# Kernel optimization log

Hardware: AMD Instinct MI355X
Metric: run time of the kernel (lower is better)

Reference implementation:

```python
import jax, jax.numpy as jnp
import numpy as np

D_MODEL, N_LAYER, VOCAB = 1024, 4, 50280
D_INNER, D_STATE, D_CONV, DT_RANK = 2048, 16, 4, 64
B, L = 1, 1024
EPS = 1e-5


def _rmsnorm(x, w):
    var = jnp.mean(jnp.square(x), axis=-1, keepdims=True)
    return x * jax.lax.rsqrt(var + EPS) * w


def _selective_scan(u, dt, A, Bm, Cm, Dv):
    # u, dt: [b,l,d]; A: [d,n]; Bm, Cm: [b,l,n]; Dv: [d]
    dA = jnp.exp(dt[..., None] * A)                      # [b,l,d,n]
    dBu = dt[..., None] * Bm[:, :, None, :] * u[..., None]  # [b,l,d,n]

    def step(s, x):
        dA_t, dBu_t, C_t = x
        s = s * dA_t + dBu_t                             # [b,d,n]
        y = jnp.einsum('bdn,bn->bd', s, C_t)
        return s, y

    s0 = jnp.zeros((u.shape[0], u.shape[2], A.shape[1]), u.dtype)
    xs = (dA.transpose(1, 0, 2, 3), dBu.transpose(1, 0, 2, 3), Cm.transpose(1, 0, 2))
    _, ys = jax.lax.scan(step, s0, xs)                   # ys: [l,b,d]
    return ys.transpose(1, 0, 2) + u * Dv


def _mixer(x, in_w, cw, cb, xp_w, dt_w, dt_b, A_log, Dv, out_w):
    Lx = x.shape[1]
    xz = jnp.einsum('bld,ed->ble', x, in_w)              # [b,l,2*d_inner]
    xp, z = jnp.split(xz, 2, axis=-1)
    # causal depthwise conv1d, kernel size D_CONV
    xpad = jnp.pad(xp, ((0, 0), (D_CONV - 1, 0), (0, 0)))
    conv = cb + sum(xpad[:, k:k + Lx, :] * cw[:, k] for k in range(D_CONV))
    u = jax.nn.silu(conv)
    xdbl = jnp.einsum('bld,ed->ble', u, xp_w)            # [b,l,dt_rank+2n]
    dt_r = xdbl[..., :DT_RANK]
    Bm = xdbl[..., DT_RANK:DT_RANK + D_STATE]
    Cm = xdbl[..., DT_RANK + D_STATE:]
    dt = jax.nn.softplus(jnp.einsum('blr,dr->bld', dt_r, dt_w) + dt_b)
    A = -jnp.exp(A_log)
    y = _selective_scan(u, dt, A, Bm, Cm, Dv)
    y = y * jax.nn.silu(z)
    return jnp.einsum('bld,ed->ble', y, out_w)


def _forward(input_ids, embedding, norm_w, in_proj_w, conv_w, conv_b, x_proj_w,
             dt_proj_w, dt_proj_b, A_log, D, out_proj_w, norm_f_w):
    hidden = embedding[input_ids]                        # [b,l,d_model]
    residual = None
    for i in range(N_LAYER):
        residual = hidden if residual is None else hidden + residual
        x = _rmsnorm(residual, norm_w[i])
        hidden = _mixer(x, in_proj_w[i], conv_w[i], conv_b[i], x_proj_w[i],
                        dt_proj_w[i], dt_proj_b[i], A_log[i], D[i], out_proj_w[i])
    residual = hidden + residual
    hf = _rmsnorm(residual, norm_f_w)
    # lm_head weight is tied to embedding
    return jnp.einsum('bld,vd->blv', hf, embedding)


def setup_inputs() -> dict:
    key = jax.random.key(0)
    ks = jax.random.split(key, 8)
    s = 0.02
    return {
        'input_ids': jax.random.randint(ks[0], (B, L), 0, VOCAB),
        'embedding': jax.random.normal(ks[1], (VOCAB, D_MODEL), jnp.float32) * s,
        'norm_w': jnp.ones((N_LAYER, D_MODEL), jnp.float32),
        'in_proj_w': jax.random.normal(ks[2], (N_LAYER, 2 * D_INNER, D_MODEL), jnp.float32) * s,
        'conv_w': jax.random.normal(ks[3], (N_LAYER, D_INNER, D_CONV), jnp.float32) * s,
        'conv_b': jnp.zeros((N_LAYER, D_INNER), jnp.float32),
        'x_proj_w': jax.random.normal(ks[4], (N_LAYER, DT_RANK + 2 * D_STATE, D_INNER), jnp.float32) * s,
        'dt_proj_w': jax.random.normal(ks[5], (N_LAYER, D_INNER, DT_RANK), jnp.float32) * s,
        'dt_proj_b': jnp.full((N_LAYER, D_INNER), -4.6, jnp.float32),  # softplus ~= 0.01
        'A_log': jnp.tile(jnp.log(jnp.arange(1.0, D_STATE + 1.0, dtype=jnp.float32))[None, None, :],
                          (N_LAYER, D_INNER, 1)),
        'D': jnp.ones((N_LAYER, D_INNER), jnp.float32),
        'out_proj_w': jax.random.normal(ks[6], (N_LAYER, D_MODEL, D_INNER), jnp.float32) * s,
        'norm_f_w': jnp.ones((D_MODEL,), jnp.float32),
    }


def reference(input_ids, embedding, norm_w, in_proj_w, conv_w, conv_b, x_proj_w,
              dt_proj_w, dt_proj_b, A_log, D, out_proj_w, norm_f_w):
    return _forward(input_ids, embedding, norm_w, in_proj_w, conv_w, conv_b,
                    x_proj_w, dt_proj_w, dt_proj_b, A_log, D, out_proj_w, norm_f_w)
```

## Files before the change

### kernel.cpp

```cpp
#include <hip/hip_runtime.h>
#include <hip/hip_bf16.h>

#define D_MODEL 1024
#define N_LAYER 4
#define D_INNER 2048
#define D_STATE 16
#define D_CONV  4
#define DT_RANK 64
#define SEQ_L   1024
#define VOCAB   50280
#define VOCAB_PAD 50304
#define NCHUNK  64
#define CLEN    16

typedef __attribute__((ext_vector_type(8))) short short8;
typedef __attribute__((ext_vector_type(4))) float f32x4;

typedef __attribute__((address_space(1))) const unsigned GUint;
typedef __attribute__((address_space(3))) unsigned LUint;

__device__ __forceinline__ float silu_f(float x) {
    return x / (1.0f + __expf(-x));
}
__device__ __forceinline__ float softplus_f(float x) {
    return fmaxf(x, 0.0f) + log1pf(__expf(-fabsf(x)));
}
__device__ __forceinline__ ushort f2bf(float f) {
    union { float f; unsigned u; } uf; uf.f = f;
    unsigned r = uf.u + 0x7FFF + ((uf.u >> 16) & 1);
    return (ushort)(r >> 16);
}

__global__ void f32_to_bf16_kernel(const float* __restrict__ in,
                                   ushort* __restrict__ out, int n4) {
    int i = blockIdx.x * 256 + threadIdx.x;
    if (i >= n4) return;
    float4 v = *(const float4*)(in + (size_t)i * 4);
    ushort4 o;
    o.x = f2bf(v.x); o.y = f2bf(v.y); o.z = f2bf(v.z); o.w = f2bf(v.w);
    *(ushort4*)(out + (size_t)i * 4) = o;
}

__global__ void xpw_convert_kernel(const float* __restrict__ src,
                                   ushort* __restrict__ dst) {
    int q = blockIdx.x * 256 + threadIdx.x;
    int layer = q / (128 * 512);
    int rq    = q % (128 * 512);
    int row   = rq / 512;
    int cq    = rq % 512;
    ushort4 o;
    if (row < 96) {
        float4 v = *(const float4*)(src + ((size_t)layer * 96 + row) * 2048 + cq * 4);
        o.x = f2bf(v.x); o.y = f2bf(v.y); o.z = f2bf(v.z); o.w = f2bf(v.w);
    } else {
        o.x = o.y = o.z = o.w = 0;
    }
    *(ushort4*)(dst + (size_t)q * 4) = o;
}

__global__ void embed_kernel(const int* __restrict__ ids,
                             const float* __restrict__ emb,
                             float* __restrict__ hidden) {
    int l = blockIdx.x;
    int t = threadIdx.x;
    int id = ids[l];
    float4 v = *(const float4*)(emb + (size_t)id * D_MODEL + t * 4);
    *(float4*)(hidden + (size_t)l * D_MODEL + t * 4) = v;
}

__global__ void add_rmsnorm_kernel(float* __restrict__ res,
                                   const float* __restrict__ part,
                                   const float* __restrict__ w,
                                   ushort* __restrict__ xout,
                                   int add, int nparts) {
    int l = blockIdx.x;
    int t = threadIdx.x;
    size_t base = (size_t)l * D_MODEL + t * 4;
    float4 r;
    if (add) r = *(const float4*)(res + base);
    else     r = make_float4(0.f, 0.f, 0.f, 0.f);
    for (int s = 0; s < nparts; ++s) {
        float4 hv = *(const float4*)(part + (size_t)s * SEQ_L * D_MODEL + base);
        r.x += hv.x; r.y += hv.y; r.z += hv.z; r.w += hv.w;
    }
    *(float4*)(res + base) = r;
    float ss = r.x * r.x + r.y * r.y + r.z * r.z + r.w * r.w;
    #pragma unroll
    for (int off = 32; off > 0; off >>= 1) ss += __shfl_down(ss, off, 64);
    __shared__ float sred[4];
    if ((t & 63) == 0) sred[t >> 6] = ss;
    __syncthreads();
    float tot = sred[0] + sred[1] + sred[2] + sred[3];
    float scale = rsqrtf(tot * (1.0f / (float)D_MODEL) + 1e-5f);
    float4 wv = *(const float4*)(w + t * 4);
    ushort4 o;
    o.x = f2bf(r.x * scale * wv.x);
    o.y = f2bf(r.y * scale * wv.y);
    o.z = f2bf(r.z * scale * wv.z);
    o.w = f2bf(r.w * scale * wv.w);
    *(ushort4*)(xout + base) = o;
}

template<int SPLIT, int EPI>
__global__ void gemm_bf16_gld_kernel(const ushort* __restrict__ A,
                                     const ushort* __restrict__ W,
                                     float* __restrict__ C,
                                     const float* __restrict__ bias,
                                     int N, int K, int lda, int ldc,
                                     int MB, int KS, int pstride) {
    __shared__ ushort As[2][128][32];
    __shared__ ushort Ws[2][128][32];
    const int t  = threadIdx.x;
    const int T  = gridDim.x >> 3;
    const int id = blockIdx.x;
    const int j  = (id & 7) * T + (id >> 3);
    const int ks  = j % KS;
    const int rem = j / KS;
    const int m0 = (rem % MB) * 128;
    const int n0 = (rem / MB) * 128;
    const int kchunk = K / KS;
    const int kbeg = ks * kchunk;
    const int kend = kbeg + kchunk;

    const int lane = t & 63;
    const int w    = t >> 6;
    const int srow = w * 16 + (lane >> 2);
    const int scol = (((lane & 3) ^ ((lane >> 3) & 3)) * 8);
    const ushort* Ag0 = A + (size_t)(m0 + srow) * lda + scol;
    const ushort* Ag1 = A + (size_t)(m0 + srow + 64) * lda + scol;
    const ushort* Wg0 = W + (size_t)(n0 + srow) * K + scol;
    const ushort* Wg1 = W + (size_t)(n0 + srow + 64) * K + scol;

    const int wm = (t >> 7) & 1;
    const int wn = (t >> 6) & 1;
    const int lr = lane & 15;
    const int lk = lane >> 4;
    const int swz = (lr >> 1) & 3;

    f32x4 acc[4][4] = {};

#define STAGE_GLD(buf, kk)                                                        \
    do {                                                                          \
        __builtin_amdgcn_global_load_lds((GUint*)(Ag0 + (kk)),                    \
            (LUint*)&As[buf][w * 16][0], 16, 0, 0);                               \
        __builtin_amdgcn_global_load_lds((GUint*)(Ag1 + (kk)),                    \
            (LUint*)&As[buf][64 + w * 16][0], 16, 0, 0);                          \
        __builtin_amdgcn_global_load_lds((GUint*)(Wg0 + (kk)),                    \
            (LUint*)&Ws[buf][w * 16][0], 16, 0, 0);                               \
        __builtin_amdgcn_global_load_lds((GUint*)(Wg1 + (kk)),                    \
            (LUint*)&Ws[buf][64 + w * 16][0], 16, 0, 0);                          \
    } while (0)

    STAGE_GLD(0, kbeg);
    int buf = 0;
    for (int k0 = kbeg;;) {
        __syncthreads();
        const bool more = (k0 + 32) < kend;
        if (more) STAGE_GLD(buf ^ 1, k0 + 32);

        short8 af[4], bfr[4];
        #pragma unroll
        for (int m = 0; m < 4; ++m)
            af[m] = *(const short8*)&As[buf][wm * 64 + m * 16 + lr][(lk ^ swz) * 8];
        #pragma unroll
        for (int n = 0; n < 4; ++n)
            bfr[n] = *(const short8*)&Ws[buf][wn * 64 + n * 16 + lr][(lk ^ swz) * 8];
        #pragma unroll
        for (int m = 0; m < 4; ++m)
            #pragma unroll
            for (int n = 0; n < 4; ++n)
                acc[m][n] = __builtin_amdgcn_mfma_f32_16x16x32_bf16(
                    af[m], bfr[n], acc[m][n], 0, 0, 0);

        if (!more) break;
        buf ^= 1;
        k0 += 32;
    }
#undef STAGE_GLD

    float* Cp = SPLIT ? (C + (size_t)ks * pstride) : C;
    #pragma unroll
    for (int m = 0; m < 4; ++m) {
        const int row = m0 + wm * 64 + m * 16 + lk * 4;
        #pragma unroll
        for (int n = 0; n < 4; ++n) {
            const int col = n0 + wn * 64 + n * 16 + lr;
            if (col < N) {
                const float bv = EPI ? bias[col] : 0.0f;
                #pragma unroll
                for (int r = 0; r < 4; ++r) {
                    float v = acc[m][n][r];
                    if (EPI) v = softplus_f(v + bv);
                    Cp[(size_t)(row + r) * ldc + col] = v;
                }
            }
        }
    }
}

__global__ void xdbl_reduce_kernel(const float* __restrict__ part,
                                   float* __restrict__ out,
                                   ushort* __restrict__ dtr_b) {
    int i = blockIdx.x * 256 + threadIdx.x;
    float4 acc = make_float4(0.f, 0.f, 0.f, 0.f);
    #pragma unroll
    for (int s = 0; s < 16; ++s) {
        float4 v = *(const float4*)(part + (size_t)s * SEQ_L * 96 + (size_t)i * 4);
        acc.x += v.x; acc.y += v.y; acc.z += v.z; acc.w += v.w;
    }
    *(float4*)(out + (size_t)i * 4) = acc;
    int c = (i * 4) % 96;
    if (c < 64) {
        int r = (i * 4) / 96;
        ushort4 o;
        o.x = f2bf(acc.x); o.y = f2bf(acc.y); o.z = f2bf(acc.z); o.w = f2bf(acc.w);
        *(ushort4*)(dtr_b + (size_t)r * 64 + c) = o;
    }
}

__global__ void conv_silu_kernel(const float* __restrict__ xz,
                                 const float* __restrict__ cw,
                                 const float* __restrict__ cb,
                                 float* __restrict__ u,
                                 ushort* __restrict__ u_b) {
    int idx = blockIdx.x * 256 + threadIdx.x;
    int l = idx >> 11;
    int c = idx & 2047;
    float acc = cb[c];
    float w0 = cw[c * 4 + 0], w1 = cw[c * 4 + 1], w2 = cw[c * 4 + 2], w3 = cw[c * 4 + 3];
    if (l >= 3) acc = fmaf(xz[(size_t)(l - 3) * 4096 + c], w0, acc);
    if (l >= 2) acc = fmaf(xz[(size_t)(l - 2) * 4096 + c], w1, acc);
    if (l >= 1) acc = fmaf(xz[(size_t)(l - 1) * 4096 + c], w2, acc);
    acc = fmaf(xz[(size_t)l * 4096 + c], w3, acc);
    float s = silu_f(acc);
    u[idx] = s;
    u_b[idx] = f2bf(s);
}

__global__ void scan_a_kernel(const float* __restrict__ u,
                              const float* __restrict__ dt,
                              const float* __restrict__ xdbl,
                              const float* __restrict__ A_log,
                              float* __restrict__ yloc,
                              float* __restrict__ cumdt,
                              float* __restrict__ s_end) {
    const int idx = blockIdx.x * 256 + threadIdx.x;
    const int d = idx & 2047;
    const int c = idx >> 11;

    float Aa[16];
    #pragma unroll
    for (int q = 0; q < 4; ++q) {
        float4 al = *(const float4*)(A_log + (size_t)d * 16 + q * 4);
        Aa[q * 4 + 0] = -__expf(al.x);
        Aa[q * 4 + 1] = -__expf(al.y);
        Aa[q * 4 + 2] = -__expf(al.z);
        Aa[q * 4 + 3] = -__expf(al.w);
    }

    float s[16];
    #pragma unroll
    for (int n = 0; n < 16; ++n) s[n] = 0.0f;
    float cd = 0.0f;

    const int l0 = c * CLEN;
    for (int i = 0; i < CLEN; ++i) {
        const int l = l0 + i;
        const float dtl = dt[(size_t)l * 2048 + d];
        const float ul  = u[(size_t)l * 2048 + d];
        float Bn[16], Cn[16];
        const float* xbp = xdbl + (size_t)l * 96;
        *(float4*)&Bn[0]  = *(const float4*)(xbp + 64);
        *(float4*)&Bn[4]  = *(const float4*)(xbp + 68);
        *(float4*)&Bn[8]  = *(const float4*)(xbp + 72);
        *(float4*)&Bn[12] = *(const float4*)(xbp + 76);
        *(float4*)&Cn[0]  = *(const float4*)(xbp + 80);
        *(float4*)&Cn[4]  = *(const float4*)(xbp + 84);
        *(float4*)&Cn[8]  = *(const float4*)(xbp + 88);
        *(float4*)&Cn[12] = *(const float4*)(xbp + 92);
        cd += dtl;
        const float dtu = dtl * ul;
        float y = 0.0f;
        #pragma unroll
        for (int n = 0; n < 16; ++n) {
            float dA = __expf(dtl * Aa[n]);
            s[n] = fmaf(s[n], dA, dtu * Bn[n]);
            y = fmaf(s[n], Cn[n], y);
        }
        yloc[(size_t)l * 4096 + d] = y;
        cumdt[(size_t)l * 2048 + d] = cd;
    }
    float* se = s_end + ((size_t)d * NCHUNK + c) * 16;
    #pragma unroll
    for (int q = 0; q < 4; ++q)
        *(float4*)(se + q * 4) = make_float4(s[q * 4], s[q * 4 + 1], s[q * 4 + 2], s[q * 4 + 3]);
}

__global__ void scan_b_kernel(const float* __restrict__ s_end,
                              const float* __restrict__ cumdt,
                              const float* __restrict__ A_log,
                              float* __restrict__ s_in) {
    const int idx = blockIdx.x * 256 + threadIdx.x;
    const int d = idx >> 4;
    const int n = idx & 15;
    const float Aa = -__expf(A_log[(size_t)d * 16 + n]);
    float s = 0.0f;
    #pragma unroll 8
    for (int c = 0; c < NCHUNK; ++c) {
        s_in[((size_t)d * NCHUNK + c) * 16 + n] = s;
        const float tot = cumdt[(size_t)(c * CLEN + CLEN - 1) * 2048 + d];
        s = s_end[((size_t)d * NCHUNK + c) * 16 + n] + __expf(Aa * tot) * s;
    }
}

__global__ void scan_c_kernel(const float* __restrict__ u,
                              const float* __restrict__ xdbl,
                              const float* __restrict__ A_log,
                              const float* __restrict__ Dv,
                              const float* __restrict__ xz,
                              const float* __restrict__ cumdt,
                              const float* __restrict__ s_in,
                              ushort* __restrict__ yb) {
    const int idx = blockIdx.x * 256 + threadIdx.x;
    const int l = idx >> 11;
    const int d = idx & 2047;
    const int c = l >> 4;

    const float cd = cumdt[idx];
    const float ul = u[idx];
    const float yv = xz[(size_t)l * 4096 + d];
    const float zv = xz[(size_t)l * 4096 + 2048 + d];
    const float* Cp = xdbl + (size_t)l * 96 + 80;
    const float* si = s_in + ((size_t)d * NCHUNK + c) * 16;

    float corr = 0.0f;
    #pragma unroll
    for (int q = 0; q < 4; ++q) {
        float4 al = *(const float4*)(A_log + (size_t)d * 16 + q * 4);
        float4 cv = *(const float4*)(Cp + q * 4);
        float4 sv = *(const float4*)(si + q * 4);
        corr = fmaf(cv.x * __expf(-__expf(al.x) * cd), sv.x, corr);
        corr = fmaf(cv.y * __expf(-__expf(al.y) * cd), sv.y, corr);
        corr = fmaf(cv.z * __expf(-__expf(al.z) * cd), sv.z, corr);
        corr = fmaf(cv.w * __expf(-__expf(al.w) * cd), sv.w, corr);
    }
    const float y = (yv + corr + Dv[d] * ul) * silu_f(zv);
    yb[idx] = f2bf(y);
}

extern "C" void kernel_launch(void* const* d_in, const int* in_sizes, int n_in,
                              void* d_out, int out_size, void* d_ws, size_t ws_size,
                              hipStream_t stream) {
    const int*   ids        = (const int*)d_in[0];
    const float* emb        = (const float*)d_in[1];
    const float* norm_w     = (const float*)d_in[2];
    const float* in_proj_w  = (const float*)d_in[3];
    const float* conv_w     = (const float*)d_in[4];
    const float* conv_b     = (const float*)d_in[5];
    const float* x_proj_w   = (const float*)d_in[6];
    const float* dt_proj_w  = (const float*)d_in[7];
    const float* dt_proj_b  = (const float*)d_in[8];
    const float* A_log      = (const float*)d_in[9];
    const float* Dv         = (const float*)d_in[10];
    const float* out_proj_w = (const float*)d_in[11];
    const float* norm_f_w   = (const float*)d_in[12];
    float* out = (float*)d_out;

    char* p = (char*)d_ws;
    ushort* emb_b  = (ushort*)p; p += (size_t)VOCAB_PAD * D_MODEL * 2;
    ushort* inw_b  = (ushort*)p; p += (size_t)N_LAYER * 4096 * 1024 * 2;
    ushort* outw_b = (ushort*)p; p += (size_t)N_LAYER * 1024 * 2048 * 2;
    ushort* xpw_b  = (ushort*)p; p += (size_t)N_LAYER * 128 * 2048 * 2;
    ushort* dtw_b  = (ushort*)p; p += (size_t)N_LAYER * 2048 * 64 * 2;
    float* residual = (float*)p; p += (size_t)SEQ_L * D_MODEL * 4;
    float* hpart    = (float*)p; p += (size_t)4 * SEQ_L * D_MODEL * 4;
    float* xdpart   = (float*)p; p += (size_t)16 * SEQ_L * 96 * 4;
    float* xdbl     = (float*)p; p += (size_t)SEQ_L * 96 * 4;
    ushort* dtr_b   = (ushort*)p; p += (size_t)SEQ_L * 64 * 2;
    ushort* xb      = (ushort*)p; p += (size_t)SEQ_L * D_MODEL * 2;
    float* xz       = (float*)p; p += (size_t)SEQ_L * 4096 * 4;
    float* u        = (float*)p; p += (size_t)SEQ_L * 2048 * 4;
    ushort* u_b     = (ushort*)p; p += (size_t)SEQ_L * 2048 * 2;
    float* dtb      = (float*)p; p += (size_t)SEQ_L * 2048 * 4;
    ushort* yb      = (ushort*)p; p += (size_t)SEQ_L * 2048 * 2;
    float* cumdt    = (float*)p; p += (size_t)SEQ_L * 2048 * 4;
    float* s_end    = (float*)p; p += (size_t)D_INNER * NCHUNK * 16 * 4;
    float* s_in     = (float*)p; p += (size_t)D_INNER * NCHUNK * 16 * 4;

    dim3 blk(256);

    f32_to_bf16_kernel<<<dim3(VOCAB * D_MODEL / 4 / 256), blk, 0, stream>>>(
        emb, emb_b, VOCAB * D_MODEL / 4);
    f32_to_bf16_kernel<<<dim3(N_LAYER * 4096 * 1024 / 4 / 256), blk, 0, stream>>>(
        in_proj_w, inw_b, N_LAYER * 4096 * 1024 / 4);
    f32_to_bf16_kernel<<<dim3(N_LAYER * 1024 * 2048 / 4 / 256), blk, 0, stream>>>(
        out_proj_w, outw_b, N_LAYER * 1024 * 2048 / 4);
    f32_to_bf16_kernel<<<dim3(N_LAYER * 2048 * 64 / 4 / 256), blk, 0, stream>>>(
        dt_proj_w, dtw_b, N_LAYER * 2048 * 64 / 4);
    xpw_convert_kernel<<<dim3(N_LAYER * 128 * 2048 / 4 / 256), blk, 0, stream>>>(
        x_proj_w, xpw_b);

    embed_kernel<<<dim3(SEQ_L), blk, 0, stream>>>(ids, emb, hpart);

    for (int i = 0; i < N_LAYER; ++i) {
        add_rmsnorm_kernel<<<dim3(SEQ_L), blk, 0, stream>>>(
            residual, hpart, norm_w + (size_t)i * D_MODEL, xb,
            i == 0 ? 0 : 1, i == 0 ? 1 : 4);

        gemm_bf16_gld_kernel<0, 0><<<dim3(256), blk, 0, stream>>>(
            xb, inw_b + (size_t)i * 4096 * 1024, xz, nullptr,
            4096, 1024, 1024, 4096, 8, 1, 0);

        conv_silu_kernel<<<dim3(SEQ_L * D_INNER / 256), blk, 0, stream>>>(
            xz, conv_w + (size_t)i * D_INNER * D_CONV, conv_b + (size_t)i * D_INNER,
            u, u_b);

        gemm_bf16_gld_kernel<1, 0><<<dim3(128), blk, 0, stream>>>(
            u_b, xpw_b + (size_t)i * 128 * 2048, xdpart, nullptr,
            96, 2048, 2048, 96, 8, 16, SEQ_L * 96);
        xdbl_reduce_kernel<<<dim3(SEQ_L * 96 / 4 / 256), blk, 0, stream>>>(
            xdpart, xdbl, dtr_b);

        gemm_bf16_gld_kernel<0, 1><<<dim3(128), blk, 0, stream>>>(
            dtr_b, dtw_b + (size_t)i * 2048 * 64, dtb,
            dt_proj_b + (size_t)i * D_INNER,
            2048, 64, 64, 2048, 8, 1, 0);

        scan_a_kernel<<<dim3(D_INNER * NCHUNK / 256), blk, 0, stream>>>(
            u, dtb, xdbl, A_log + (size_t)i * D_INNER * D_STATE, xz, cumdt, s_end);
        scan_b_kernel<<<dim3(D_INNER * 16 / 256), blk, 0, stream>>>(
            s_end, cumdt, A_log + (size_t)i * D_INNER * D_STATE, s_in);
        scan_c_kernel<<<dim3(SEQ_L * D_INNER / 256), blk, 0, stream>>>(
            u, xdbl, A_log + (size_t)i * D_INNER * D_STATE,
            Dv + (size_t)i * D_INNER, xz, cumdt, s_in, yb);

        gemm_bf16_gld_kernel<1, 0><<<dim3(256), blk, 0, stream>>>(
            yb, outw_b + (size_t)i * 1024 * 2048, hpart, nullptr,
            1024, 2048, 2048, 1024, 8, 4, SEQ_L * D_MODEL);
    }

    add_rmsnorm_kernel<<<dim3(SEQ_L), blk, 0, stream>>>(
        residual, hpart, norm_f_w, xb, 1, 4);

    gemm_bf16_gld_kernel<0, 0><<<dim3(3144), blk, 0, stream>>>(
        xb, emb_b, out, nullptr, VOCAB, 1024, 1024, VOCAB, 8, 1, 0);
}
```

Before: 822.2 us.

## Store xz, u and local scan outputs in bf16; widen scan chunks

The in_proj GEMM now writes xz in bf16 instead of fp32, and the fp32 copy of u is dropped so downstream kernels read u_b. scan_a writes its local y output into the bf16 xz buffer. The conv kernel is vectorised to handle 8 channels per thread with short8 loads. The scan chunk count is halved while chunk length doubles. The aim is to cut memory traffic across the per-layer elementwise and scan kernels, at the cost of extra rounding in u, z and the local scan output, and fewer parallel threads in scan_a.

```diff
diff --git a/kernel.cpp b/kernel.cpp
--- a/kernel.cpp
+++ b/kernel.cpp
@@ -10,8 +10,8 @@
 #define SEQ_L   1024
 #define VOCAB   50280
 #define VOCAB_PAD 50304
-#define NCHUNK  64
-#define CLEN    16
+#define NCHUNK  32
+#define CLEN    32
 
 typedef __attribute__((ext_vector_type(8))) short short8;
 typedef __attribute__((ext_vector_type(4))) float f32x4;
@@ -29,6 +29,9 @@
     union { float f; unsigned u; } uf; uf.f = f;
     unsigned r = uf.u + 0x7FFF + ((uf.u >> 16) & 1);
     return (ushort)(r >> 16);
+}
+__device__ __forceinline__ float bf2f(ushort u) {
+    union { unsigned u; float f; } x; x.u = ((unsigned)u) << 16; return x.f;
 }
 
 __global__ void f32_to_bf16_kernel(const float* __restrict__ in,
@@ -101,10 +104,10 @@
     *(ushort4*)(xout + base) = o;
 }
 
-template<int SPLIT, int EPI>
+template<int SPLIT, int OUTB, int EPI>
 __global__ void gemm_bf16_gld_kernel(const ushort* __restrict__ A,
                                      const ushort* __restrict__ W,
-                                     float* __restrict__ C,
+                                     void* __restrict__ Cv,
                                      const float* __restrict__ bias,
                                      int N, int K, int lda, int ldc,
                                      int MB, int KS, int pstride) {
@@ -178,7 +181,9 @@
     }
 #undef STAGE_GLD
 
-    float* Cp = SPLIT ? (C + (size_t)ks * pstride) : C;
+    const size_t poff = SPLIT ? (size_t)ks * pstride : 0;
+    float*  Cf = (float*)Cv + poff;
+    ushort* Cb = (ushort*)Cv + poff;
     #pragma unroll
     for (int m = 0; m < 4; ++m) {
         const int row = m0 + wm * 64 + m * 16 + lk * 4;
@@ -191,7 +196,10 @@
                 for (int r = 0; r < 4; ++r) {
                     float v = acc[m][n][r];
                     if (EPI) v = softplus_f(v + bv);
-                    Cp[(size_t)(row + r) * ldc + col] = v;
+                    if (OUTB)
+                        Cb[(size_t)(row + r) * ldc + col] = f2bf(v);
+                    else
+                        Cf[(size_t)(row + r) * ldc + col] = v;
                 }
             }
         }
@@ -218,30 +226,44 @@
     }
 }
 
-__global__ void conv_silu_kernel(const float* __restrict__ xz,
+__global__ void conv_silu_kernel(const ushort* __restrict__ xz,
                                  const float* __restrict__ cw,
                                  const float* __restrict__ cb,
-                                 float* __restrict__ u,
                                  ushort* __restrict__ u_b) {
-    int idx = blockIdx.x * 256 + threadIdx.x;
-    int l = idx >> 11;
-    int c = idx & 2047;
-    float acc = cb[c];
-    float w0 = cw[c * 4 + 0], w1 = cw[c * 4 + 1], w2 = cw[c * 4 + 2], w3 = cw[c * 4 + 3];
-    if (l >= 3) acc = fmaf(xz[(size_t)(l - 3) * 4096 + c], w0, acc);
-    if (l >= 2) acc = fmaf(xz[(size_t)(l - 2) * 4096 + c], w1, acc);
-    if (l >= 1) acc = fmaf(xz[(size_t)(l - 1) * 4096 + c], w2, acc);
-    acc = fmaf(xz[(size_t)l * 4096 + c], w3, acc);
-    float s = silu_f(acc);
-    u[idx] = s;
-    u_b[idx] = f2bf(s);
-}
-
-__global__ void scan_a_kernel(const float* __restrict__ u,
+    int idx8 = blockIdx.x * 256 + threadIdx.x;
+    int l  = idx8 >> 8;
+    int c0 = (idx8 & 255) * 8;
+
+    float4 w4[8];
+    float acc[8];
+    #pragma unroll
+    for (int e = 0; e < 8; ++e) {
+        w4[e] = *(const float4*)(cw + (size_t)(c0 + e) * 4);
+        acc[e] = cb[c0 + e];
+    }
+    #pragma unroll
+    for (int k = 0; k < 4; ++k) {
+        int ls = l - (3 - k);
+        if (ls < 0) continue;
+        short8 pv = *(const short8*)(xz + (size_t)ls * 4096 + c0);
+        #pragma unroll
+        for (int e = 0; e < 8; ++e) {
+            float wk = (k == 0) ? w4[e].x : (k == 1) ? w4[e].y
+                     : (k == 2) ? w4[e].z : w4[e].w;
+            acc[e] = fmaf(bf2f((ushort)pv[e]), wk, acc[e]);
+        }
+    }
+    short8 o;
+    #pragma unroll
+    for (int e = 0; e < 8; ++e) o[e] = (short)f2bf(silu_f(acc[e]));
+    *(short8*)(u_b + (size_t)l * 2048 + c0) = o;
+}
+
+__global__ void scan_a_kernel(const ushort* __restrict__ u_b,
                               const float* __restrict__ dt,
                               const float* __restrict__ xdbl,
                               const float* __restrict__ A_log,
-                              float* __restrict__ yloc,
+                              ushort* __restrict__ yloc,
                               float* __restrict__ cumdt,
                               float* __restrict__ s_end) {
     const int idx = blockIdx.x * 256 + threadIdx.x;
@@ -267,7 +289,7 @@
     for (int i = 0; i < CLEN; ++i) {
         const int l = l0 + i;
         const float dtl = dt[(size_t)l * 2048 + d];
-        const float ul  = u[(size_t)l * 2048 + d];
+        const float ul  = bf2f(u_b[(size_t)l * 2048 + d]);
         float Bn[16], Cn[16];
         const float* xbp = xdbl + (size_t)l * 96;
         *(float4*)&Bn[0]  = *(const float4*)(xbp + 64);
@@ -287,7 +309,7 @@
             s[n] = fmaf(s[n], dA, dtu * Bn[n]);
             y = fmaf(s[n], Cn[n], y);
         }
-        yloc[(size_t)l * 4096 + d] = y;
+        yloc[(size_t)l * 4096 + d] = f2bf(y);
         cumdt[(size_t)l * 2048 + d] = cd;
     }
     float* se = s_end + ((size_t)d * NCHUNK + c) * 16;
@@ -305,7 +327,7 @@
     const int n = idx & 15;
     const float Aa = -__expf(A_log[(size_t)d * 16 + n]);
     float s = 0.0f;
-    #pragma unroll 8
+    #pragma unroll
     for (int c = 0; c < NCHUNK; ++c) {
         s_in[((size_t)d * NCHUNK + c) * 16 + n] = s;
         const float tot = cumdt[(size_t)(c * CLEN + CLEN - 1) * 2048 + d];
@@ -313,23 +335,23 @@
     }
 }
 
-__global__ void scan_c_kernel(const float* __restrict__ u,
+__global__ void scan_c_kernel(const ushort* __restrict__ u_b,
                               const float* __restrict__ xdbl,
                               const float* __restrict__ A_log,
                               const float* __restrict__ Dv,
-                              const float* __restrict__ xz,
+                              const ushort* __restrict__ xz,
                               const float* __restrict__ cumdt,
                               const float* __restrict__ s_in,
                               ushort* __restrict__ yb) {
     const int idx = blockIdx.x * 256 + threadIdx.x;
     const int l = idx >> 11;
     const int d = idx & 2047;
-    const int c = l >> 4;
+    const int c = l >> 5;
 
     const float cd = cumdt[idx];
-    const float ul = u[idx];
-    const float yv = xz[(size_t)l * 4096 + d];
-    const float zv = xz[(size_t)l * 4096 + 2048 + d];
+    const float ul = bf2f(u_b[idx]);
+    const float yv = bf2f(xz[(size_t)l * 4096 + d]);
+    const float zv = bf2f(xz[(size_t)l * 4096 + 2048 + d]);
     const float* Cp = xdbl + (size_t)l * 96 + 80;
     const float* si = s_in + ((size_t)d * NCHUNK + c) * 16;
 
@@ -378,8 +400,7 @@
     float* xdbl     = (float*)p; p += (size_t)SEQ_L * 96 * 4;
     ushort* dtr_b   = (ushort*)p; p += (size_t)SEQ_L * 64 * 2;
     ushort* xb      = (ushort*)p; p += (size_t)SEQ_L * D_MODEL * 2;
-    float* xz       = (float*)p; p += (size_t)SEQ_L * 4096 * 4;
-    float* u        = (float*)p; p += (size_t)SEQ_L * 2048 * 4;
+    ushort* xzb     = (ushort*)p; p += (size_t)SEQ_L * 4096 * 2;
     ushort* u_b     = (ushort*)p; p += (size_t)SEQ_L * 2048 * 2;
     float* dtb      = (float*)p; p += (size_t)SEQ_L * 2048 * 4;
     ushort* yb      = (ushort*)p; p += (size_t)SEQ_L * 2048 * 2;
@@ -407,34 +428,34 @@
             residual, hpart, norm_w + (size_t)i * D_MODEL, xb,
             i == 0 ? 0 : 1, i == 0 ? 1 : 4);
 
-        gemm_bf16_gld_kernel<0, 0><<<dim3(256), blk, 0, stream>>>(
-            xb, inw_b + (size_t)i * 4096 * 1024, xz, nullptr,
+        gemm_bf16_gld_kernel<0, 1, 0><<<dim3(256), blk, 0, stream>>>(
+            xb, inw_b + (size_t)i * 4096 * 1024, xzb, nullptr,
             4096, 1024, 1024, 4096, 8, 1, 0);
 
-        conv_silu_kernel<<<dim3(SEQ_L * D_INNER / 256), blk, 0, stream>>>(
-            xz, conv_w + (size_t)i * D_INNER * D_CONV, conv_b + (size_t)i * D_INNER,
-            u, u_b);
-
-        gemm_bf16_gld_kernel<1, 0><<<dim3(128), blk, 0, stream>>>(
+        conv_silu_kernel<<<dim3(SEQ_L * D_INNER / 8 / 256), blk, 0, stream>>>(
+            xzb, conv_w + (size_t)i * D_INNER * D_CONV, conv_b + (size_t)i * D_INNER,
+            u_b);
+
+        gemm_bf16_gld_kernel<1, 0, 0><<<dim3(128), blk, 0, stream>>>(
             u_b, xpw_b + (size_t)i * 128 * 2048, xdpart, nullptr,
             96, 2048, 2048, 96, 8, 16, SEQ_L * 96);
         xdbl_reduce_kernel<<<dim3(SEQ_L * 96 / 4 / 256), blk, 0, stream>>>(
             xdpart, xdbl, dtr_b);
 
-        gemm_bf16_gld_kernel<0, 1><<<dim3(128), blk, 0, stream>>>(
+        gemm_bf16_gld_kernel<0, 0, 1><<<dim3(128), blk, 0, stream>>>(
             dtr_b, dtw_b + (size_t)i * 2048 * 64, dtb,
             dt_proj_b + (size_t)i * D_INNER,
             2048, 64, 64, 2048, 8, 1, 0);
 
         scan_a_kernel<<<dim3(D_INNER * NCHUNK / 256), blk, 0, stream>>>(
-            u, dtb, xdbl, A_log + (size_t)i * D_INNER * D_STATE, xz, cumdt, s_end);
+            u_b, dtb, xdbl, A_log + (size_t)i * D_INNER * D_STATE, xzb, cumdt, s_end);
         scan_b_kernel<<<dim3(D_INNER * 16 / 256), blk, 0, stream>>>(
             s_end, cumdt, A_log + (size_t)i * D_INNER * D_STATE, s_in);
         scan_c_kernel<<<dim3(SEQ_L * D_INNER / 256), blk, 0, stream>>>(
-            u, xdbl, A_log + (size_t)i * D_INNER * D_STATE,
-            Dv + (size_t)i * D_INNER, xz, cumdt, s_in, yb);
-
-        gemm_bf16_gld_kernel<1, 0><<<dim3(256), blk, 0, stream>>>(
+            u_b, xdbl, A_log + (size_t)i * D_INNER * D_STATE,
+            Dv + (size_t)i * D_INNER, xzb, cumdt, s_in, yb);
+
+        gemm_bf16_gld_kernel<1, 0, 0><<<dim3(256), blk, 0, stream>>>(
             yb, outw_b + (size_t)i * 1024 * 2048, hpart, nullptr,
             1024, 2048, 2048, 1024, 8, 4, SEQ_L * D_MODEL);
     }
@@ -442,6 +463,6 @@
     add_rmsnorm_kernel<<<dim3(SEQ_L), blk, 0, stream>>>(
         residual, hpart, norm_f_w, xb, 1, 4);
 
-    gemm_bf16_gld_kernel<0, 0><<<dim3(3144), blk, 0, stream>>>(
+    gemm_bf16_gld_kernel<0, 0, 0><<<dim3(3144), blk, 0, stream>>>(
         xb, emb_b, out, nullptr, VOCAB, 1024, 1024, VOCAB, 8, 1, 0);
 }
```

New measurement: 848.3 us. 1.03x slower.
